# Kernel optimization log

Hardware: AMD Instinct MI355X
Metric: run time of the kernel (lower is better)

Reference implementation:

```python
import jax, jax.numpy as jnp
import numpy as np

G, N = 1024, 40            # graphs, nodes per graph (complete graphs)
SLOPE = 0.1                # leaky relu negative slope
SMAT_IDX = jnp.array([0, 1, 2, 3, 1, 4, 5, 6, 2, 5, 7, 8, 3, 6, 8, 9])


def setup_inputs() -> dict:
    key = jax.random.key(0)
    ks = jax.random.split(key, 24)

    # --- graph structure: G identical complete graphs of N nodes ---
    ii, jj = np.meshgrid(np.arange(N), np.arange(N), indexing="ij")
    mask = ii != jj
    src_l, dst_l = ii[mask], jj[mask]              # directed edges per graph
    offs = (np.arange(G) * N)[:, None]
    edge_index = np.stack([(src_l[None] + offs).ravel(),
                           (dst_l[None] + offs).ravel()]).astype(np.int64)
    iu, ju = np.triu_indices(N, 1)
    M = iu.shape[0]                                 # 780 undirected edges
    ud_edges = np.stack([iu, ju], 1).astype(np.int64)
    edge_map = np.zeros((N, N), np.int64)
    edge_map[iu, ju] = np.arange(M)
    edge_map[ju, iu] = np.arange(M)

    def w(k, shape, fan_in):
        return jax.random.normal(k, shape, jnp.float32) / np.sqrt(fan_in)

    inp = {
        "x": jax.random.normal(ks[0], (G * N, 16), jnp.float32),
        "edge_index": jnp.asarray(edge_index),
        "ud_edges": jnp.asarray(ud_edges),
        "edge_map": jnp.asarray(edge_map),
        # GCN stack 6->32->32->64
        "Wg0": w(ks[1], (6, 32), 6),   "bg0": jnp.zeros((32,), jnp.float32),
        "Wg1": w(ks[2], (32, 32), 32), "bg1": jnp.zeros((32,), jnp.float32),
        "Wg2": w(ks[3], (32, 64), 32), "bg2": jnp.zeros((64,), jnp.float32),
        # node MLP 64->64->64->10
        "Wn0": w(ks[4], (64, 64), 64), "bn0": jnp.zeros((64,), jnp.float32),
        "Wn1": w(ks[5], (64, 64), 64), "bn1": jnp.zeros((64,), jnp.float32),
        "Wn2": w(ks[6], (64, 10), 64), "bn2": jnp.zeros((10,), jnp.float32),
        # edge MLP 64->64->64->10
        "We0": w(ks[7], (64, 64), 64), "be0": jnp.zeros((64,), jnp.float32),
        "We1": w(ks[8], (64, 64), 64), "be1": jnp.zeros((64,), jnp.float32),
        "We2": w(ks[9], (64, 10), 64), "be2": jnp.zeros((10,), jnp.float32),
    }
    return inp


def _forward(x, edge_index, ud_edges, edge_map,
             Wg0, bg0, Wg1, bg1, Wg2, bg2,
             Wn0, bn0, Wn1, bn1, Wn2, bn2,
             We0, be0, We1, be1, We2, be2):
    num_nodes = x.shape[0]
    h = x[:, :6]                                   # node_feature_mode == 1
    src, dst = edge_index[0], edge_index[1]

    # GCN normalization (add_self_loops=False, edge_weight=1)
    deg = jax.ops.segment_sum(jnp.ones(src.shape[0], x.dtype), dst,
                              num_segments=num_nodes)
    dis = jnp.where(deg > 0, jax.lax.rsqrt(jnp.maximum(deg, 1e-12)), 0.0)
    norm = dis[src] * dis[dst]                     # [E]

    def gcn(h, W, b):
        m = (h @ W)[src] * norm[:, None]
        return jax.ops.segment_sum(m, dst, num_segments=num_nodes) + b

    # eval mode: dropout is identity
    h = jax.nn.leaky_relu(gcn(h, Wg0, bg0), SLOPE)
    h = jax.nn.leaky_relu(gcn(h, Wg1, bg1), SLOPE)
    h = gcn(h, Wg2, bg2)                           # [G*N, 64]

    hg = h.reshape(G, N, -1)                       # [G, N, 64]

    def mlp(z, Ws, bs):
        for W, b in zip(Ws[:-1], bs[:-1]):
            z = jax.nn.leaky_relu(z @ W + b, SLOPE)
        return z @ Ws[-1] + bs[-1]

    vp = mlp(hg, [Wn0, Wn1, Wn2], [bn0, bn1, bn2])            # [G, N, 10]
    e = hg[:, ud_edges[:, 0], :] + hg[:, ud_edges[:, 1], :]   # [G, M, 64]
    ep = mlp(e, [We0, We1, We2], [be0, be1, be2])             # [G, M, 10]

    # recover_X: diag blocks smat(vp[i]), off-diag smat(ep[edge_map[i,j]])
    epm = ep[:, edge_map, :]                                  # [G, N, N, 10]
    eye = jnp.eye(N, dtype=bool)[None, :, :, None]
    vecs = jnp.where(eye, vp[:, :, None, :], epm)             # [G, N, N, 10]
    blocks = vecs[..., SMAT_IDX].reshape(G, N, N, 4, 4)
    X = blocks.transpose(0, 1, 3, 2, 4).reshape(G, 4 * N, 4 * N)
    return h, X


def reference(x, edge_index, ud_edges, edge_map,
              Wg0, bg0, Wg1, bg1, Wg2, bg2,
              Wn0, bn0, Wn1, bn1, Wn2, bn2,
              We0, be0, We1, be1, We2, be2):
    return _forward(x, edge_index, ud_edges, edge_map,
                    Wg0, bg0, Wg1, bg1, Wg2, bg2,
                    Wn0, bn0, Wn1, bn1, Wn2, bn2,
                    We0, be0, We1, be1, We2, be2)
```

## Files before the change

kernel.cpp:

```cpp
#include <hip/hip_runtime.h>

#define G_GRAPHS 1024
#define N_NODES  40
#define M_EDGES  780
#define NUM_NODES (G_GRAPHS * N_NODES)
#define H_ELEMS  (NUM_NODES * 64)
#define X_STRIDE 160
#define X_PER_G  25600
#define SLOPE 0.1f

#define EDGE_BLOCKS 6240
#define VP_BLOCKS   320
#define PACK_PER_MLP 9216

typedef __bf16 bf16x8 __attribute__((ext_vector_type(8)));
typedef unsigned short us8 __attribute__((ext_vector_type(8)));
typedef float f32x4 __attribute__((ext_vector_type(4)));

__device__ __forceinline__ float lrelu(float v) { return fmaxf(v, SLOPE * v); }
__device__ __forceinline__ unsigned short f2bf(float x) {
    __bf16 b = (__bf16)x;
    return __builtin_bit_cast(unsigned short, b);
}

__global__ __launch_bounds__(256) void k_prep(const float* __restrict__ We0,
                                              const float* __restrict__ We1,
                                              const float* __restrict__ We2,
                                              const float* __restrict__ Wn0,
                                              const float* __restrict__ Wn1,
                                              const float* __restrict__ Wn2,
                                              unsigned short* __restrict__ wp) {
    int t = blockIdx.x * 256 + threadIdx.x;
    int mlp = t / PACK_PER_MLP;
    int o = t - mlp * PACK_PER_MLP;
    const float* W0 = mlp ? Wn0 : We0;
    const float* W1 = mlp ? Wn1 : We1;
    const float* W2 = mlp ? Wn2 : We2;
    float val;
    if (o < 8192) {
        const float* W = (o < 4096) ? W0 : W1;
        int idx = o & 4095;
        int j = idx & 7, l = (idx >> 3) & 63, tt = idx >> 9;
        int kt = tt & 1, nt = tt >> 1;
        int k = kt * 32 + ((l >> 4) & 3) * 8 + j;
        int n = nt * 16 + (l & 15);
        val = W[k * 64 + n];
    } else {
        int idx = o - 8192;
        int j = idx & 7, l = (idx >> 3) & 63, kt = idx >> 9;
        int k = kt * 32 + ((l >> 4) & 3) * 8 + j;
        int n = l & 15;
        val = (n < 10) ? W2[k * 10 + n] : 0.f;
    }
    wp[mlp * PACK_PER_MLP + o] = f2bf(val);
}

__global__ __launch_bounds__(256) void k_gcn(const float* __restrict__ x,
                                             const float* __restrict__ Wg0,
                                             const float* __restrict__ bg0,
                                             const float* __restrict__ Wg1,
                                             const float* __restrict__ bg1,
                                             const float* __restrict__ Wg2,
                                             const float* __restrict__ bg2,
                                             float* __restrict__ hout) {
    __shared__ float h0[N_NODES * 6];
    __shared__ float buf[N_NODES * 64];
    __shared__ float S[64];
    __shared__ float P[8 * 64];
    __shared__ float h1[N_NODES * 32];
    __shared__ float h2[N_NODES * 32];

    const int g = blockIdx.x;
    const int tid = threadIdx.x;
    const float inv39 = 1.0f / 39.0f;

    for (int idx = tid; idx < N_NODES * 6; idx += 256) {
        int n = idx / 6, f = idx - n * 6;
        h0[idx] = x[(g * N_NODES + n) * 16 + f];
    }
    __syncthreads();

    for (int idx = tid; idx < N_NODES * 32; idx += 256) {
        int n = idx >> 5, c = idx & 31;
        float s = 0.f;
#pragma unroll
        for (int f = 0; f < 6; f++) s += h0[n * 6 + f] * Wg0[f * 32 + c];
        buf[n * 32 + c] = s;
    }
    __syncthreads();
    { int c = tid & 31, grp = tid >> 5; float s = 0.f;
#pragma unroll
      for (int n = grp * 5; n < grp * 5 + 5; n++) s += buf[n * 32 + c];
      P[grp * 32 + c] = s; }
    __syncthreads();
    if (tid < 32) { float s = 0.f;
#pragma unroll
      for (int grp = 0; grp < 8; grp++) s += P[grp * 32 + tid];
      S[tid] = s; }
    __syncthreads();
    for (int idx = tid; idx < N_NODES * 32; idx += 256) {
        int n = idx >> 5, c = idx & 31;
        h1[idx] = lrelu((S[c] - buf[n * 32 + c]) * inv39 + bg0[c]);
    }
    __syncthreads();

    for (int idx = tid; idx < N_NODES * 32; idx += 256) {
        int n = idx >> 5, c = idx & 31;
        float s = 0.f;
#pragma unroll
        for (int m = 0; m < 32; m++) s += h1[n * 32 + m] * Wg1[m * 32 + c];
        buf[n * 32 + c] = s;
    }
    __syncthreads();
    { int c = tid & 31, grp = tid >> 5; float s = 0.f;
#pragma unroll
      for (int n = grp * 5; n < grp * 5 + 5; n++) s += buf[n * 32 + c];
      P[grp * 32 + c] = s; }
    __syncthreads();
    if (tid < 32) { float s = 0.f;
#pragma unroll
      for (int grp = 0; grp < 8; grp++) s += P[grp * 32 + tid];
      S[tid] = s; }
    __syncthreads();
    for (int idx = tid; idx < N_NODES * 32; idx += 256) {
        int n = idx >> 5, c = idx & 31;
        h2[idx] = lrelu((S[c] - buf[n * 32 + c]) * inv39 + bg1[c]);
    }
    __syncthreads();

    for (int idx = tid; idx < N_NODES * 64; idx += 256) {
        int n = idx >> 6, c = idx & 63;
        float s = 0.f;
#pragma unroll
        for (int m = 0; m < 32; m++) s += h2[n * 32 + m] * Wg2[m * 64 + c];
        buf[idx] = s;
    }
    __syncthreads();
    { int c = tid & 63, grp = tid >> 6; float s = 0.f;
#pragma unroll
      for (int n = grp * 10; n < grp * 10 + 10; n++) s += buf[n * 64 + c];
      P[grp * 64 + c] = s; }
    __syncthreads();
    if (tid < 64) { float s = 0.f;
#pragma unroll
      for (int grp = 0; grp < 4; grp++) s += P[grp * 64 + tid];
      S[tid] = s; }
    __syncthreads();
    for (int idx = tid; idx < N_NODES * 64; idx += 256) {
        int n = idx >> 6, c = idx & 63;
        hout[(g * N_NODES + n) * 64 + c] = (S[c] - buf[n * 64 + c]) * inv39 + bg2[c];
    }
}

__global__ __launch_bounds__(256) void k_mlp(const float* __restrict__ h,
                                             const unsigned short* __restrict__ wp,
                                             const float* __restrict__ be0,
                                             const float* __restrict__ be1,
                                             const float* __restrict__ be2,
                                             const float* __restrict__ bn0,
                                             const float* __restrict__ bn1,
                                             const float* __restrict__ bn2,
                                             float* __restrict__ X) {
    __shared__ __align__(16) unsigned short sE[128 * 64];
    __shared__ __align__(16) unsigned short sZ[128 * 64];
    __shared__ __align__(16) float sEP[128 * 12];

    const int tid = threadIdx.x;
    const int l = tid & 63;
    const int w = tid >> 6;
    const int bid = blockIdx.x;
    const bool is_edge = (bid < EDGE_BLOCKS);

    const unsigned short* wb = wp + (is_edge ? 0 : PACK_PER_MLP);
    const float* b0 = is_edge ? be0 : bn0;
    const float* b1 = is_edge ? be1 : bn1;
    const float* b2 = is_edge ? be2 : bn2;

    const int r = 32 * w + (l >> 1);
    const int hf = l & 1;
    int g, i = 0, j = 0;
    if (is_edge) {
        int eid = bid * 128 + r;
        g = eid / M_EDGES;
        int m = eid - g * M_EDGES;
        int rem = m;
        while (rem >= (N_NODES - 1) - i) { rem -= (N_NODES - 1) - i; ++i; }
        j = i + 1 + rem;
    } else {
        int nid = (bid - EDGE_BLOCKS) * 128 + r;
        g = nid / N_NODES;
        i = nid - g * N_NODES;
        j = i;
    }

    {
        const float4* pa = (const float4*)(h + (g * N_NODES + i) * 64 + hf * 32);
        const float4* pb = (const float4*)(h + (g * N_NODES + j) * 64 + hf * 32);
        unsigned short tmp[32];
#pragma unroll
        for (int q = 0; q < 8; q++) {
            float4 a = pa[q];
            if (is_edge) {
                float4 b = pb[q];
                a.x += b.x; a.y += b.y; a.z += b.z; a.w += b.w;
            }
            tmp[4 * q + 0] = f2bf(a.x); tmp[4 * q + 1] = f2bf(a.y);
            tmp[4 * q + 2] = f2bf(a.z); tmp[4 * q + 3] = f2bf(a.w);
        }
#pragma unroll
        for (int q = 0; q < 4; q++) {
            int cs = (hf * 4 + q) ^ (r & 7);
            *(us8*)((char*)sE + r * 128 + cs * 16) = *(const us8*)(tmp + 8 * q);
        }
    }

    const int col0 = l & 15, rq = (l >> 4) & 3;

    auto Afrag = [&](const unsigned short* s, int mt, int kt) -> bf16x8 {
        int row = 32 * w + mt * 16 + col0;
        int cs = (kt * 4 + rq) ^ (row & 7);
        return __builtin_bit_cast(bf16x8,
            *(const us8*)((const char*)s + row * 128 + cs * 16));
    };
    auto Bfrag = [&](const unsigned short* base, int tt) -> bf16x8 {
        return __builtin_bit_cast(bf16x8, *(const us8*)(base + (tt * 64 + l) * 8));
    };

    {
        bf16x8 A[2][2];
#pragma unroll
        for (int mt = 0; mt < 2; mt++)
#pragma unroll
            for (int kt = 0; kt < 2; kt++) A[mt][kt] = Afrag(sE, mt, kt);
        f32x4 acc[2][4];
#pragma unroll
        for (int mt = 0; mt < 2; mt++)
#pragma unroll
            for (int nt = 0; nt < 4; nt++) acc[mt][nt] = (f32x4){0.f, 0.f, 0.f, 0.f};
#pragma unroll
        for (int nt = 0; nt < 4; nt++) {
            bf16x8 B0 = Bfrag(wb, nt * 2 + 0), B1 = Bfrag(wb, nt * 2 + 1);
#pragma unroll
            for (int mt = 0; mt < 2; mt++) {
                acc[mt][nt] = __builtin_amdgcn_mfma_f32_16x16x32_bf16(A[mt][0], B0, acc[mt][nt], 0, 0, 0);
                acc[mt][nt] = __builtin_amdgcn_mfma_f32_16x16x32_bf16(A[mt][1], B1, acc[mt][nt], 0, 0, 0);
            }
        }
#pragma unroll
        for (int nt = 0; nt < 4; nt++) {
            float bi = b0[nt * 16 + col0];
#pragma unroll
            for (int mt = 0; mt < 2; mt++)
#pragma unroll
                for (int reg = 0; reg < 4; reg++) {
                    int row = 32 * w + mt * 16 + rq * 4 + reg;
                    int col = nt * 16 + col0;
                    float z = lrelu(acc[mt][nt][reg] + bi);
                    int cs = (col >> 3) ^ (row & 7);
                    *(unsigned short*)((char*)sZ + row * 128 + cs * 16 + (col & 7) * 2) = f2bf(z);
                }
        }
    }

    {
        bf16x8 A[2][2];
#pragma unroll
        for (int mt = 0; mt < 2; mt++)
#pragma unroll
            for (int kt = 0; kt < 2; kt++) A[mt][kt] = Afrag(sZ, mt, kt);
        f32x4 acc[2][4];
#pragma unroll
        for (int mt = 0; mt < 2; mt++)
#pragma unroll
            for (int nt = 0; nt < 4; nt++) acc[mt][nt] = (f32x4){0.f, 0.f, 0.f, 0.f};
        const unsigned short* w1p = wb + 4096;
#pragma unroll
        for (int nt = 0; nt < 4; nt++) {
            bf16x8 B0 = Bfrag(w1p, nt * 2 + 0), B1 = Bfrag(w1p, nt * 2 + 1);
#pragma unroll
            for (int mt = 0; mt < 2; mt++) {
                acc[mt][nt] = __builtin_amdgcn_mfma_f32_16x16x32_bf16(A[mt][0], B0, acc[mt][nt], 0, 0, 0);
                acc[mt][nt] = __builtin_amdgcn_mfma_f32_16x16x32_bf16(A[mt][1], B1, acc[mt][nt], 0, 0, 0);
            }
        }
#pragma unroll
        for (int nt = 0; nt < 4; nt++) {
            float bi = b1[nt * 16 + col0];
#pragma unroll
            for (int mt = 0; mt < 2; mt++)
#pragma unroll
                for (int reg = 0; reg < 4; reg++) {
                    int row = 32 * w + mt * 16 + rq * 4 + reg;
                    int col = nt * 16 + col0;
                    float z = lrelu(acc[mt][nt][reg] + bi);
                    int cs = (col >> 3) ^ (row & 7);
                    *(unsigned short*)((char*)sE + row * 128 + cs * 16 + (col & 7) * 2) = f2bf(z);
                }
        }
    }

    {
        bf16x8 A[2][2];
#pragma unroll
        for (int mt = 0; mt < 2; mt++)
#pragma unroll
            for (int kt = 0; kt < 2; kt++) A[mt][kt] = Afrag(sE, mt, kt);
        const unsigned short* w2p = wb + 8192;
        bf16x8 B0 = Bfrag(w2p, 0), B1 = Bfrag(w2p, 1);
        f32x4 acc[2];
#pragma unroll
        for (int mt = 0; mt < 2; mt++) {
            acc[mt] = (f32x4){0.f, 0.f, 0.f, 0.f};
            acc[mt] = __builtin_amdgcn_mfma_f32_16x16x32_bf16(A[mt][0], B0, acc[mt], 0, 0, 0);
            acc[mt] = __builtin_amdgcn_mfma_f32_16x16x32_bf16(A[mt][1], B1, acc[mt], 0, 0, 0);
        }
        if (col0 < 10) {
            float bz = b2[col0];
#pragma unroll
            for (int mt = 0; mt < 2; mt++)
#pragma unroll
                for (int reg = 0; reg < 4; reg++) {
                    int row = 32 * w + mt * 16 + rq * 4 + reg;
                    sEP[row * 12 + col0] = acc[mt][reg] + bz;
                }
        }
    }

    {
        const float4* ev = (const float4*)(sEP + r * 12);
        float4 e0 = ev[0], e1 = ev[1], e2 = ev[2];
        float4 r0 = make_float4(e0.x, e0.y, e0.z, e0.w);
        float4 r1 = make_float4(e0.y, e1.x, e1.y, e1.z);
        float4 r2 = make_float4(e0.z, e1.y, e1.w, e2.x);
        float4 r3 = make_float4(e0.w, e1.z, e2.x, e2.y);
        float* Xg = X + g * X_PER_G;
        if (is_edge) {
            int bi = hf ? j : i, bj = hf ? i : j;
            float* p = Xg + (4 * bi) * X_STRIDE + 4 * bj;
            *(float4*)(p + 0 * X_STRIDE) = r0;
            *(float4*)(p + 1 * X_STRIDE) = r1;
            *(float4*)(p + 2 * X_STRIDE) = r2;
            *(float4*)(p + 3 * X_STRIDE) = r3;
        } else {
            float* p = Xg + (4 * i + hf * 2) * X_STRIDE + 4 * i;
            if (hf == 0) {
                *(float4*)(p + 0 * X_STRIDE) = r0;
                *(float4*)(p + 1 * X_STRIDE) = r1;
            } else {
                *(float4*)(p + 0 * X_STRIDE) = r2;
                *(float4*)(p + 1 * X_STRIDE) = r3;
            }
        }
    }
}

extern "C" void kernel_launch(void* const* d_in, const int* in_sizes, int n_in,
                              void* d_out, int out_size, void* d_ws, size_t ws_size,
                              hipStream_t stream) {
    const float* x   = (const float*)d_in[0];
    const float* Wg0 = (const float*)d_in[4];
    const float* bg0 = (const float*)d_in[5];
    const float* Wg1 = (const float*)d_in[6];
    const float* bg1 = (const float*)d_in[7];
    const float* Wg2 = (const float*)d_in[8];
    const float* bg2 = (const float*)d_in[9];
    const float* Wn0 = (const float*)d_in[10];
    const float* bn0 = (const float*)d_in[11];
    const float* Wn1 = (const float*)d_in[12];
    const float* bn1 = (const float*)d_in[13];
    const float* Wn2 = (const float*)d_in[14];
    const float* bn2 = (const float*)d_in[15];
    const float* We0 = (const float*)d_in[16];
    const float* be0 = (const float*)d_in[17];
    const float* We1 = (const float*)d_in[18];
    const float* be1 = (const float*)d_in[19];
    const float* We2 = (const float*)d_in[20];
    const float* be2 = (const float*)d_in[21];

    float* hout = (float*)d_out;
    float* X    = hout + H_ELEMS;
    unsigned short* wp = (unsigned short*)d_ws;

    k_prep<<<72, 256, 0, stream>>>(We0, We1, We2, Wn0, Wn1, Wn2, wp);
    k_gcn<<<G_GRAPHS, 256, 0, stream>>>(x, Wg0, bg0, Wg1, bg1, Wg2, bg2, hout);
    k_mlp<<<EDGE_BLOCKS + VP_BLOCKS, 256, 0, stream>>>(hout, wp,
                                                       be0, be1, be2,
                                                       bn0, bn1, bn2, X);
}
```

Measured before the change: 239.6 us.

## Map one graph per wavefront in GCN kernel using register-held features and shuffles

The GCN kernel is restructured so that each 64-lane wavefront handles one graph, with one node per lane. Node features live in registers, and the per-channel sums over neighbours are done with xor-shuffle reductions instead of shared memory and many block barriers. The launch drops to a quarter as many blocks. In exchange, 24 of 64 lanes sit idle, each lane runs about 64 serial shuffle reductions per layer, and register pressure is high with possible spills.

```diff
diff --git a/kernel.cpp b/kernel.cpp
--- a/kernel.cpp
+++ b/kernel.cpp
@@ -63,92 +63,86 @@
                                              const float* __restrict__ Wg2,
                                              const float* __restrict__ bg2,
                                              float* __restrict__ hout) {
-    __shared__ float h0[N_NODES * 6];
-    __shared__ float buf[N_NODES * 64];
-    __shared__ float S[64];
-    __shared__ float P[8 * 64];
-    __shared__ float h1[N_NODES * 32];
-    __shared__ float h2[N_NODES * 32];
-
-    const int g = blockIdx.x;
-    const int tid = threadIdx.x;
+    const int lane = threadIdx.x & 63;
+    const int wv   = threadIdx.x >> 6;
+    const int g    = blockIdx.x * 4 + wv;
+    const int n    = lane;
+    const bool act = (n < N_NODES);
     const float inv39 = 1.0f / 39.0f;
 
-    for (int idx = tid; idx < N_NODES * 6; idx += 256) {
-        int n = idx / 6, f = idx - n * 6;
-        h0[idx] = x[(g * N_NODES + n) * 16 + f];
-    }
-    __syncthreads();
-
-    for (int idx = tid; idx < N_NODES * 32; idx += 256) {
-        int n = idx >> 5, c = idx & 31;
-        float s = 0.f;
-#pragma unroll
-        for (int f = 0; f < 6; f++) s += h0[n * 6 + f] * Wg0[f * 32 + c];
-        buf[n * 32 + c] = s;
-    }
-    __syncthreads();
-    { int c = tid & 31, grp = tid >> 5; float s = 0.f;
-#pragma unroll
-      for (int n = grp * 5; n < grp * 5 + 5; n++) s += buf[n * 32 + c];
-      P[grp * 32 + c] = s; }
-    __syncthreads();
-    if (tid < 32) { float s = 0.f;
-#pragma unroll
-      for (int grp = 0; grp < 8; grp++) s += P[grp * 32 + tid];
-      S[tid] = s; }
-    __syncthreads();
-    for (int idx = tid; idx < N_NODES * 32; idx += 256) {
-        int n = idx >> 5, c = idx & 31;
-        h1[idx] = lrelu((S[c] - buf[n * 32 + c]) * inv39 + bg0[c]);
-    }
-    __syncthreads();
-
-    for (int idx = tid; idx < N_NODES * 32; idx += 256) {
-        int n = idx >> 5, c = idx & 31;
-        float s = 0.f;
-#pragma unroll
-        for (int m = 0; m < 32; m++) s += h1[n * 32 + m] * Wg1[m * 32 + c];
-        buf[n * 32 + c] = s;
-    }
-    __syncthreads();
-    { int c = tid & 31, grp = tid >> 5; float s = 0.f;
-#pragma unroll
-      for (int n = grp * 5; n < grp * 5 + 5; n++) s += buf[n * 32 + c];
-      P[grp * 32 + c] = s; }
-    __syncthreads();
-    if (tid < 32) { float s = 0.f;
-#pragma unroll
-      for (int grp = 0; grp < 8; grp++) s += P[grp * 32 + tid];
-      S[tid] = s; }
-    __syncthreads();
-    for (int idx = tid; idx < N_NODES * 32; idx += 256) {
-        int n = idx >> 5, c = idx & 31;
-        h2[idx] = lrelu((S[c] - buf[n * 32 + c]) * inv39 + bg1[c]);
-    }
-    __syncthreads();
-
-    for (int idx = tid; idx < N_NODES * 64; idx += 256) {
-        int n = idx >> 6, c = idx & 63;
-        float s = 0.f;
-#pragma unroll
-        for (int m = 0; m < 32; m++) s += h2[n * 32 + m] * Wg2[m * 64 + c];
-        buf[idx] = s;
-    }
-    __syncthreads();
-    { int c = tid & 63, grp = tid >> 6; float s = 0.f;
-#pragma unroll
-      for (int n = grp * 10; n < grp * 10 + 10; n++) s += buf[n * 64 + c];
-      P[grp * 64 + c] = s; }
-    __syncthreads();
-    if (tid < 64) { float s = 0.f;
-#pragma unroll
-      for (int grp = 0; grp < 4; grp++) s += P[grp * 64 + tid];
-      S[tid] = s; }
-    __syncthreads();
-    for (int idx = tid; idx < N_NODES * 64; idx += 256) {
-        int n = idx >> 6, c = idx & 63;
-        hout[(g * N_NODES + n) * 64 + c] = (S[c] - buf[n * 64 + c]) * inv39 + bg2[c];
+    float h0[6];
+#pragma unroll
+    for (int f = 0; f < 6; f++) h0[f] = 0.f;
+    if (act) {
+        const float* xr = x + (g * N_NODES + n) * 16;
+#pragma unroll
+        for (int f = 0; f < 6; f++) h0[f] = xr[f];
+    }
+
+    float h1[32];
+    {
+        float z[32];
+#pragma unroll
+        for (int c = 0; c < 32; c++) {
+            float s = 0.f;
+#pragma unroll
+            for (int f = 0; f < 6; f++) s += h0[f] * Wg0[f * 32 + c];
+            z[c] = s;
+        }
+#pragma unroll
+        for (int c = 0; c < 32; c++) {
+            float own = z[c], s = own;
+#pragma unroll
+            for (int st = 1; st < 64; st <<= 1) s += __shfl_xor(s, st, 64);
+            float v = (s - own) * inv39 + bg0[c];
+            h1[c] = act ? lrelu(v) : 0.f;
+        }
+    }
+
+    float h2[32];
+    {
+        float z[32];
+#pragma unroll
+        for (int c = 0; c < 32; c++) {
+            float s = 0.f;
+#pragma unroll
+            for (int m = 0; m < 32; m++) s += h1[m] * Wg1[m * 32 + c];
+            z[c] = s;
+        }
+#pragma unroll
+        for (int c = 0; c < 32; c++) {
+            float own = z[c], s = own;
+#pragma unroll
+            for (int st = 1; st < 64; st <<= 1) s += __shfl_xor(s, st, 64);
+            float v = (s - own) * inv39 + bg1[c];
+            h2[c] = act ? lrelu(v) : 0.f;
+        }
+    }
+
+#pragma unroll
+    for (int half = 0; half < 2; half++) {
+        float z[32];
+#pragma unroll
+        for (int c = 0; c < 32; c++) {
+            float s = 0.f;
+#pragma unroll
+            for (int m = 0; m < 32; m++) s += h2[m] * Wg2[m * 64 + half * 32 + c];
+            z[c] = s;
+        }
+#pragma unroll
+        for (int c = 0; c < 32; c++) {
+            float own = z[c], s = own;
+#pragma unroll
+            for (int st = 1; st < 64; st <<= 1) s += __shfl_xor(s, st, 64);
+            z[c] = (s - own) * inv39 + bg2[half * 32 + c];
+        }
+        if (act) {
+            float4* dst = (float4*)(hout + (g * N_NODES + n) * 64 + half * 32);
+#pragma unroll
+            for (int q = 0; q < 8; q++)
+                dst[q] = make_float4(z[4 * q + 0], z[4 * q + 1],
+                                     z[4 * q + 2], z[4 * q + 3]);
+        }
     }
 }
 
@@ -382,7 +376,7 @@
     unsigned short* wp = (unsigned short*)d_ws;
 
     k_prep<<<72, 256, 0, stream>>>(We0, We1, We2, Wn0, Wn1, Wn2, wp);
-    k_gcn<<<G_GRAPHS, 256, 0, stream>>>(x, Wg0, bg0, Wg1, bg1, Wg2, bg2, hout);
+    k_gcn<<<G_GRAPHS / 4, 256, 0, stream>>>(x, Wg0, bg0, Wg1, bg1, Wg2, bg2, hout);
     k_mlp<<<EDGE_BLOCKS + VP_BLOCKS, 256, 0, stream>>>(hout, wp,
                                                        be0, be1, be2,
                                                        bn0, bn1, bn2, X);
```

Result: slower. 327.8 us (+36.8%).

## Swap MFMA operand roles so weights are A and activations B, packing outputs

Applied to the files above, without the earlier changes.

The MLP matmuls are transposed: packed weights become the A operand and node/edge activations the B operand. Each lane's accumulator then holds four consecutive output features, so bias loads become one float4 and hidden activations are written to LDS as packed bf16 pairs (one 8-byte store) instead of scalar 2-byte stores. The final-layer output is staged per wave in the reused sZ buffer, removing a separate LDS array. This cuts LDS store instructions and LDS footprint, at the cost of a changed swizzle and a different per-wave staging layout that must still match the row mapping.

```diff
diff --git a/kernel.cpp b/kernel.cpp
--- a/kernel.cpp
+++ b/kernel.cpp
@@ -21,6 +21,9 @@
 __device__ __forceinline__ unsigned short f2bf(float x) {
     __bf16 b = (__bf16)x;
     return __builtin_bit_cast(unsigned short, b);
+}
+__device__ __forceinline__ unsigned int pk2bf(float a, float b) {
+    return (unsigned int)f2bf(a) | ((unsigned int)f2bf(b) << 16);
 }
 
 __global__ __launch_bounds__(256) void k_prep(const float* __restrict__ We0,
@@ -41,16 +44,16 @@
         const float* W = (o < 4096) ? W0 : W1;
         int idx = o & 4095;
         int j = idx & 7, l = (idx >> 3) & 63, tt = idx >> 9;
-        int kt = tt & 1, nt = tt >> 1;
+        int kt = tt & 1, mt = tt >> 1;
         int k = kt * 32 + ((l >> 4) & 3) * 8 + j;
-        int n = nt * 16 + (l & 15);
-        val = W[k * 64 + n];
+        int m = mt * 16 + (l & 15);
+        val = W[k * 64 + m];
     } else {
         int idx = o - 8192;
         int j = idx & 7, l = (idx >> 3) & 63, kt = idx >> 9;
         int k = kt * 32 + ((l >> 4) & 3) * 8 + j;
-        int n = l & 15;
-        val = (n < 10) ? W2[k * 10 + n] : 0.f;
+        int m = l & 15;
+        val = (m < 10) ? W2[k * 10 + m] : 0.f;
     }
     wp[mlp * PACK_PER_MLP + o] = f2bf(val);
 }
@@ -163,7 +166,6 @@
                                              float* __restrict__ X) {
     __shared__ __align__(16) unsigned short sE[128 * 64];
     __shared__ __align__(16) unsigned short sZ[128 * 64];
-    __shared__ __align__(16) float sEP[128 * 12];
 
     const int tid = threadIdx.x;
     const int l = tid & 63;
@@ -214,121 +216,105 @@
         }
     }
 
-    const int col0 = l & 15, rq = (l >> 4) & 3;
-
-    auto Afrag = [&](const unsigned short* s, int mt, int kt) -> bf16x8 {
-        int row = 32 * w + mt * 16 + col0;
-        int cs = (kt * 4 + rq) ^ (row & 7);
+    const int nl = l & 15;
+    const int rq = (l >> 4) & 3;
+
+    auto WA = [&](const unsigned short* base, int mt, int kt) -> bf16x8 {
         return __builtin_bit_cast(bf16x8,
-            *(const us8*)((const char*)s + row * 128 + cs * 16));
+            *(const us8*)(base + ((mt * 2 + kt) * 64 + l) * 8));
     };
-    auto Bfrag = [&](const unsigned short* base, int tt) -> bf16x8 {
-        return __builtin_bit_cast(bf16x8, *(const us8*)(base + (tt * 64 + l) * 8));
+    auto ZB = [&](const unsigned short* s, int nt, int kt) -> bf16x8 {
+        int node = 32 * w + nt * 16 + nl;
+        int cs = (kt * 4 + rq) ^ (node & 7);
+        return __builtin_bit_cast(bf16x8,
+            *(const us8*)((const char*)s + node * 128 + cs * 16));
     };
-
-    {
-        bf16x8 A[2][2];
-#pragma unroll
-        for (int mt = 0; mt < 2; mt++)
-#pragma unroll
-            for (int kt = 0; kt < 2; kt++) A[mt][kt] = Afrag(sE, mt, kt);
-        f32x4 acc[2][4];
-#pragma unroll
-        for (int mt = 0; mt < 2; mt++)
-#pragma unroll
-            for (int nt = 0; nt < 4; nt++) acc[mt][nt] = (f32x4){0.f, 0.f, 0.f, 0.f};
-#pragma unroll
-        for (int nt = 0; nt < 4; nt++) {
-            bf16x8 B0 = Bfrag(wb, nt * 2 + 0), B1 = Bfrag(wb, nt * 2 + 1);
-#pragma unroll
-            for (int mt = 0; mt < 2; mt++) {
-                acc[mt][nt] = __builtin_amdgcn_mfma_f32_16x16x32_bf16(A[mt][0], B0, acc[mt][nt], 0, 0, 0);
-                acc[mt][nt] = __builtin_amdgcn_mfma_f32_16x16x32_bf16(A[mt][1], B1, acc[mt][nt], 0, 0, 0);
+    auto zstore = [&](unsigned short* s, int mt, int nt, const f32x4& v) {
+        int node = 32 * w + nt * 16 + nl;
+        int cs = (mt * 2 + (rq >> 1)) ^ (node & 7);
+        uint2 u = make_uint2(pk2bf(v[0], v[1]), pk2bf(v[2], v[3]));
+        *(uint2*)((char*)s + node * 128 + cs * 16 + (rq & 1) * 8) = u;
+    };
+
+    {
+        bf16x8 B[2][2];
+#pragma unroll
+        for (int nt = 0; nt < 2; nt++)
+#pragma unroll
+            for (int kt = 0; kt < 2; kt++) B[nt][kt] = ZB(sE, nt, kt);
+#pragma unroll
+        for (int mt = 0; mt < 4; mt++) {
+            bf16x8 A0 = WA(wb, mt, 0), A1 = WA(wb, mt, 1);
+            float4 bv = *(const float4*)(b0 + mt * 16 + rq * 4);
+#pragma unroll
+            for (int nt = 0; nt < 2; nt++) {
+                f32x4 acc = (f32x4){0.f, 0.f, 0.f, 0.f};
+                acc = __builtin_amdgcn_mfma_f32_16x16x32_bf16(A0, B[nt][0], acc, 0, 0, 0);
+                acc = __builtin_amdgcn_mfma_f32_16x16x32_bf16(A1, B[nt][1], acc, 0, 0, 0);
+                f32x4 z;
+                z[0] = lrelu(acc[0] + bv.x); z[1] = lrelu(acc[1] + bv.y);
+                z[2] = lrelu(acc[2] + bv.z); z[3] = lrelu(acc[3] + bv.w);
+                zstore(sZ, mt, nt, z);
             }
         }
-#pragma unroll
-        for (int nt = 0; nt < 4; nt++) {
-            float bi = b0[nt * 16 + col0];
-#pragma unroll
-            for (int mt = 0; mt < 2; mt++)
-#pragma unroll
-                for (int reg = 0; reg < 4; reg++) {
-                    int row = 32 * w + mt * 16 + rq * 4 + reg;
-                    int col = nt * 16 + col0;
-                    float z = lrelu(acc[mt][nt][reg] + bi);
-                    int cs = (col >> 3) ^ (row & 7);
-                    *(unsigned short*)((char*)sZ + row * 128 + cs * 16 + (col & 7) * 2) = f2bf(z);
-                }
-        }
-    }
-
-    {
-        bf16x8 A[2][2];
-#pragma unroll
-        for (int mt = 0; mt < 2; mt++)
-#pragma unroll
-            for (int kt = 0; kt < 2; kt++) A[mt][kt] = Afrag(sZ, mt, kt);
-        f32x4 acc[2][4];
-#pragma unroll
-        for (int mt = 0; mt < 2; mt++)
-#pragma unroll
-            for (int nt = 0; nt < 4; nt++) acc[mt][nt] = (f32x4){0.f, 0.f, 0.f, 0.f};
+    }
+
+    {
+        bf16x8 B[2][2];
+#pragma unroll
+        for (int nt = 0; nt < 2; nt++)
+#pragma unroll
+            for (int kt = 0; kt < 2; kt++) B[nt][kt] = ZB(sZ, nt, kt);
         const unsigned short* w1p = wb + 4096;
 #pragma unroll
-        for (int nt = 0; nt < 4; nt++) {
-            bf16x8 B0 = Bfrag(w1p, nt * 2 + 0), B1 = Bfrag(w1p, nt * 2 + 1);
-#pragma unroll
-            for (int mt = 0; mt < 2; mt++) {
-                acc[mt][nt] = __builtin_amdgcn_mfma_f32_16x16x32_bf16(A[mt][0], B0, acc[mt][nt], 0, 0, 0);
-                acc[mt][nt] = __builtin_amdgcn_mfma_f32_16x16x32_bf16(A[mt][1], B1, acc[mt][nt], 0, 0, 0);
+        for (int mt = 0; mt < 4; mt++) {
+            bf16x8 A0 = WA(w1p, mt, 0), A1 = WA(w1p, mt, 1);
+            float4 bv = *(const float4*)(b1 + mt * 16 + rq * 4);
+#pragma unroll
+            for (int nt = 0; nt < 2; nt++) {
+                f32x4 acc = (f32x4){0.f, 0.f, 0.f, 0.f};
+                acc = __builtin_amdgcn_mfma_f32_16x16x32_bf16(A0, B[nt][0], acc, 0, 0, 0);
+                acc = __builtin_amdgcn_mfma_f32_16x16x32_bf16(A1, B[nt][1], acc, 0, 0, 0);
+                f32x4 z;
+                z[0] = lrelu(acc[0] + bv.x); z[1] = lrelu(acc[1] + bv.y);
+                z[2] = lrelu(acc[2] + bv.z); z[3] = lrelu(acc[3] + bv.w);
+                zstore(sE, mt, nt, z);
             }
         }
-#pragma unroll
-        for (int nt = 0; nt < 4; nt++) {
-            float bi = b1[nt * 16 + col0];
-#pragma unroll
-            for (int mt = 0; mt < 2; mt++)
-#pragma unroll
-                for (int reg = 0; reg < 4; reg++) {
-                    int row = 32 * w + mt * 16 + rq * 4 + reg;
-                    int col = nt * 16 + col0;
-                    float z = lrelu(acc[mt][nt][reg] + bi);
-                    int cs = (col >> 3) ^ (row & 7);
-                    *(unsigned short*)((char*)sE + row * 128 + cs * 16 + (col & 7) * 2) = f2bf(z);
-                }
-        }
-    }
-
-    {
-        bf16x8 A[2][2];
-#pragma unroll
-        for (int mt = 0; mt < 2; mt++)
-#pragma unroll
-            for (int kt = 0; kt < 2; kt++) A[mt][kt] = Afrag(sE, mt, kt);
+    }
+
+    float* sEPf = (float*)sZ + w * 1024;
+    {
+        bf16x8 B[2][2];
+#pragma unroll
+        for (int nt = 0; nt < 2; nt++)
+#pragma unroll
+            for (int kt = 0; kt < 2; kt++) B[nt][kt] = ZB(sE, nt, kt);
         const unsigned short* w2p = wb + 8192;
-        bf16x8 B0 = Bfrag(w2p, 0), B1 = Bfrag(w2p, 1);
-        f32x4 acc[2];
-#pragma unroll
-        for (int mt = 0; mt < 2; mt++) {
-            acc[mt] = (f32x4){0.f, 0.f, 0.f, 0.f};
-            acc[mt] = __builtin_amdgcn_mfma_f32_16x16x32_bf16(A[mt][0], B0, acc[mt], 0, 0, 0);
-            acc[mt] = __builtin_amdgcn_mfma_f32_16x16x32_bf16(A[mt][1], B1, acc[mt], 0, 0, 0);
-        }
-        if (col0 < 10) {
-            float bz = b2[col0];
-#pragma unroll
-            for (int mt = 0; mt < 2; mt++)
-#pragma unroll
-                for (int reg = 0; reg < 4; reg++) {
-                    int row = 32 * w + mt * 16 + rq * 4 + reg;
-                    sEP[row * 12 + col0] = acc[mt][reg] + bz;
-                }
-        }
-    }
-
-    {
-        const float4* ev = (const float4*)(sEP + r * 12);
-        float4 e0 = ev[0], e1 = ev[1], e2 = ev[2];
+        bf16x8 A0 = WA(w2p, 0, 0), A1 = WA(w2p, 0, 1);
+        float bz[4];
+#pragma unroll
+        for (int k = 0; k < 4; k++) {
+            int f = rq * 4 + k;
+            bz[k] = (f < 10) ? b2[f] : 0.f;
+        }
+#pragma unroll
+        for (int nt = 0; nt < 2; nt++) {
+            f32x4 acc = (f32x4){0.f, 0.f, 0.f, 0.f};
+            acc = __builtin_amdgcn_mfma_f32_16x16x32_bf16(A0, B[nt][0], acc, 0, 0, 0);
+            acc = __builtin_amdgcn_mfma_f32_16x16x32_bf16(A1, B[nt][1], acc, 0, 0, 0);
+            int nl2 = nt * 16 + nl;
+            float4 v = make_float4(acc[0] + bz[0], acc[1] + bz[1],
+                                   acc[2] + bz[2], acc[3] + bz[3]);
+            *(float4*)(sEPf + nl2 * 20 + rq * 4) = v;
+        }
+    }
+
+    {
+        const float* ep = sEPf + (r & 31) * 20;
+        float4 e0 = *(const float4*)(ep + 0);
+        float4 e1 = *(const float4*)(ep + 4);
+        float4 e2 = *(const float4*)(ep + 8);
         float4 r0 = make_float4(e0.x, e0.y, e0.z, e0.w);
         float4 r1 = make_float4(e0.y, e1.x, e1.y, e1.z);
         float4 r2 = make_float4(e0.z, e1.y, e1.w, e2.x);
```

Measured after the change: 235.9 us. No clear change (-1.6%).
